# Performance work log

Hardware: AMD Instinct MI355X
Metric: run time of the kernel (lower is better)

Reference implementation:

```python
import jax, jax.numpy as jnp
import numpy as np

L1_PENALTY = 0.01
RHO = 5.0
N_ITERS = 100  # fixed iteration count standing in for max_iter=2000 w/ tol
EPS = 1e-12


def _normalize(x):
    # matches torch.nn.functional.normalize(dim=1, eps=1e-12)
    n = jnp.linalg.norm(x, axis=-1, keepdims=True)
    return x / jnp.maximum(n, EPS)


def _admm_nnlasso(D, Y, lam, rho, n_iters):
    """Batched nonnegative Lasso via ADMM.
    Solves per-row: min_w 0.5*||D^T w - y||^2 + lam*||w||_1, w >= 0.
    D: [c, d] dictionary, Y: [B, d] targets. Returns W: [B, c].
    x-update uses Woodbury: (A^T A + rho I)^{-1} b = (b - A^T (G + rho I)^{-1} A b)/rho
    with A = D^T, G = A A^T = D^T D ([d, d], d=512 -> cheap Cholesky).
    """
    d = D.shape[1]
    G = D.T @ D + rho * jnp.eye(d, dtype=D.dtype)  # [d, d]
    cf = jax.scipy.linalg.cho_factor(G)
    Aty = Y @ D.T  # [B, c] = A^T y batched
    thr = lam / rho

    def step(carry, _):
        z, u = carry
        b = Aty + rho * (z - u)               # [B, c]
        s = jax.scipy.linalg.cho_solve(cf, (b @ D).T).T  # [B, d]
        x = (b - s @ D.T) / rho               # [B, c]
        z_new = jnp.maximum(x + u - thr, 0.0)  # nonneg soft-threshold
        u_new = u + x - z_new
        return (z_new, u_new), None

    z0 = jnp.zeros_like(Aty)
    (z, _), _ = jax.lax.scan(step, (z0, z0), None, length=n_iters)
    return z


def setup_inputs() -> dict:
    key = jax.random.key(0)
    k1, k2, k3, k4 = jax.random.split(key, 4)
    B, C, Dm = 1024, 10000, 512
    image = jax.random.normal(k1, (B, Dm), dtype=jnp.float32)
    text = jax.random.normal(k2, (B, Dm), dtype=jnp.float32)
    image_mean = 0.1 * jax.random.normal(k3, (Dm,), dtype=jnp.float32)
    dictionary = jax.random.normal(k4, (C, Dm), dtype=jnp.float32)
    dictionary = dictionary / jnp.linalg.norm(dictionary, axis=1, keepdims=True)
    return {"image": image, "text": text, "image_mean": image_mean,
            "dictionary": dictionary}


def reference(image, text, image_mean, dictionary):
    # encode_image
    img = _normalize(image)
    centered = _normalize(img - image_mean)
    weights = _admm_nnlasso(dictionary, centered, L1_PENALTY, RHO, N_ITERS)
    recon = weights @ dictionary           # [B, d]
    recon = _normalize(recon)
    recon = _normalize(recon + image_mean)
    # encode_text (decomp_text=False -> just normalize)
    txt = _normalize(text)
    return recon, txt
```

## Files before the change

### kernel.cpp

```cpp
#include <hip/hip_runtime.h>
#include <cstddef>
#include <cstdint>

#define BDIM  1024
#define DM    512
#define CREAL 10000
#define CP    10112
#define KSPL  16
#define RHOC  5.0f
#define THRC  (0.01f/5.0f)
#define NIT   100
#define NSIT  12

typedef float f32x4 __attribute__((ext_vector_type(4)));
typedef _Float16 f16x8 __attribute__((ext_vector_type(8)));


__device__ __forceinline__ f16x8 scl6(f16x8 v) {
    f16x8 r;
#pragma unroll
    for (int i = 0; i < 8; i++) r[i] = v[i] * (_Float16)0.015625f;
    return r;
}

__device__ __forceinline__ float blk_sum256(float v) {
    __shared__ float sb[4];
#pragma unroll
    for (int o = 32; o; o >>= 1) v += __shfl_down(v, o, 64);
    int lane = threadIdx.x & 63, w = threadIdx.x >> 6;
    __syncthreads();
    if (lane == 0) sb[w] = v;
    __syncthreads();
    return sb[0] + sb[1] + sb[2] + sb[3];
}

__global__ __launch_bounds__(256) void knorm_rows(const float* __restrict__ X,
                                                  float* __restrict__ out) {
    int row = blockIdx.x, t = threadIdx.x;
    int off = row * DM + t * 2;
    float2 v = *(const float2*)(X + off);
    float ss = blk_sum256(v.x * v.x + v.y * v.y);
    float inv = 1.0f / fmaxf(sqrtf(ss), 1e-12f);
    float2 o = {v.x * inv, v.y * inv};
    *(float2*)(out + off) = o;
}

__global__ __launch_bounds__(256) void kprep_Y(const float* __restrict__ img,
                                               const float* __restrict__ mean,
                                               float* __restrict__ Y) {
    int row = blockIdx.x, t = threadIdx.x;
    int off = row * DM + t * 2;
    float2 v = *(const float2*)(img + off);
    float ss = blk_sum256(v.x * v.x + v.y * v.y);
    float inv = 1.0f / fmaxf(sqrtf(ss), 1e-12f);
    float2 mm = *(const float2*)(mean + t * 2);
    float tx = v.x * inv - mm.x, ty = v.y * inv - mm.y;
    float ss2 = blk_sum256(tx * tx + ty * ty);
    float inv2 = 1.0f / fmaxf(sqrtf(ss2), 1e-12f);
    float2 o = {tx * inv2, ty * inv2};
    *(float2*)(Y + off) = o;
}

__global__ __launch_bounds__(256) void ktrs(const float* __restrict__ in,
                                            float* __restrict__ out32,
                                            _Float16* __restrict__ oH,
                                            _Float16* __restrict__ oL,
                                            int Rvalid, int Cin, int Rout) {
    __shared__ float tile[64][65];
    int r0 = blockIdx.x * 64;
    int c0 = blockIdx.y * 64;
    int t = threadIdx.x;
    int ri = r0 + (t >> 2);
    int cc = (t & 3) * 16;
#pragma unroll
    for (int q = 0; q < 4; ++q) {
        float4 v = {0.f, 0.f, 0.f, 0.f};
        if (ri < Rvalid) v = *(const float4*)(in + (size_t)ri * Cin + c0 + cc + q * 4);
        *(float4*)&tile[t >> 2][cc + q * 4] = v;
    }
    __syncthreads();
    int oc = c0 + (t >> 2);
    int orr = r0 + (t & 3) * 16;
    _Float16 hv[16], lv[16];
#pragma unroll
    for (int q = 0; q < 16; ++q) {
        float v = tile[(t & 3) * 16 + q][t >> 2];
        _Float16 h = (_Float16)v;
        _Float16 l = (_Float16)((v - (float)h) * 64.f);
        hv[q] = h; lv[q] = l;
        if (out32) out32[(size_t)oc * Rout + orr + q] = (float)h + (float)l * 0.015625f;
    }
    int rt = oc >> 4, rin = oc & 15;
    int kt = orr >> 5;
    int kq0 = (orr >> 3) & 3;
    size_t base = ((size_t)rt * (Rout >> 5) + kt) * 512;
    *(f16x8*)(oH + base + (size_t)(kq0 * 16 + rin) * 8)       = *(f16x8*)&hv[0];
    *(f16x8*)(oH + base + (size_t)((kq0 + 1) * 16 + rin) * 8) = *(f16x8*)&hv[8];
    *(f16x8*)(oL + base + (size_t)(kq0 * 16 + rin) * 8)       = *(f16x8*)&lv[0];
    *(f16x8*)(oL + base + (size_t)((kq0 + 1) * 16 + rin) * 8) = *(f16x8*)&lv[8];
}

__global__ __launch_bounds__(256) void kG(const float* __restrict__ Dt,
                                          float* __restrict__ G) {
    __shared__ float As[32][68];
    __shared__ float Bs[32][68];
    int tid = threadIdx.x;
    int j0 = blockIdx.x * 64, i0 = blockIdx.y * 64;
    int tn = (tid & 15) * 4, tm = (tid >> 4) * 4;
    float acc[4][4];
#pragma unroll
    for (int i = 0; i < 4; i++)
#pragma unroll
        for (int j = 0; j < 4; j++) acc[i][j] = 0.f;
    for (int k0 = 0; k0 < CP; k0 += 32) {
        __syncthreads();
#pragma unroll
        for (int p = 0; p < 2; ++p) {
            int idx = tid + p * 256;
            int row = idx >> 3, kv = (idx & 7) << 2;
            float4 va = *(const float4*)(Dt + (size_t)(i0 + row) * CP + k0 + kv);
            As[kv + 0][row] = va.x; As[kv + 1][row] = va.y;
            As[kv + 2][row] = va.z; As[kv + 3][row] = va.w;
            float4 vb = *(const float4*)(Dt + (size_t)(j0 + row) * CP + k0 + kv);
            Bs[kv + 0][row] = vb.x; Bs[kv + 1][row] = vb.y;
            Bs[kv + 2][row] = vb.z; Bs[kv + 3][row] = vb.w;
        }
        __syncthreads();
#pragma unroll
        for (int k = 0; k < 32; ++k) {
            float4 a4 = *(const float4*)&As[k][tm];
            float4 b4 = *(const float4*)&Bs[k][tn];
            float af[4] = {a4.x, a4.y, a4.z, a4.w};
            float bf[4] = {b4.x, b4.y, b4.z, b4.w};
#pragma unroll
            for (int i = 0; i < 4; i++)
#pragma unroll
                for (int j = 0; j < 4; j++) acc[i][j] = fmaf(af[i], bf[j], acc[i][j]);
        }
    }
#pragma unroll
    for (int i = 0; i < 4; i++)
#pragma unroll
        for (int j = 0; j < 4; j++) {
            int gi = i0 + tm + i, gj = j0 + tn + j;
            G[gi * DM + gj] = acc[i][j] + ((gi == gj) ? RHOC : 0.f);
        }
}

__global__ void krow_abssum(const float* __restrict__ G, float* __restrict__ gmax) {
    int row = blockIdx.x, t = threadIdx.x;
    float s = 0.f;
    for (int j = t; j < DM; j += 64) s += fabsf(G[row * DM + j]);
#pragma unroll
    for (int o = 32; o; o >>= 1) s += __shfl_down(s, o, 64);
    if (t == 0) atomicMax((int*)gmax, __float_as_int(s));
}

__global__ void kinit_X0(const float* __restrict__ gmax, float* __restrict__ X) {
    int idx = blockIdx.x * 256 + threadIdx.x;
    int i = idx >> 9, j = idx & 511;
    X[idx] = (i == j) ? (1.0f / gmax[0]) : 0.0f;
}

__global__ __launch_bounds__(256) void kgemm_ns_T(const float* __restrict__ G,
                                                  const float* __restrict__ X,
                                                  float* __restrict__ T) {
    __shared__ float As[32][68];
    __shared__ float Bs[32][68];
    int tid = threadIdx.x;
    int n0 = blockIdx.x * 64, m0 = blockIdx.y * 64;
    int tn = (tid & 15) * 4, tm = (tid >> 4) * 4;
    float acc[4][4];
#pragma unroll
    for (int i = 0; i < 4; i++)
#pragma unroll
        for (int j = 0; j < 4; j++) acc[i][j] = 0.f;
    for (int k0 = 0; k0 < DM; k0 += 32) {
        __syncthreads();
#pragma unroll
        for (int p = 0; p < 2; ++p) {
            int idx = tid + p * 256;
            {
                int row = idx >> 3, kv = (idx & 7) << 2;
                float4 v = *(const float4*)(G + (m0 + row) * DM + k0 + kv);
                As[kv + 0][row] = v.x; As[kv + 1][row] = v.y;
                As[kv + 2][row] = v.z; As[kv + 3][row] = v.w;
            }
            {
                int r = idx >> 4, cv = (idx & 15) << 2;
                *(float4*)&Bs[r][cv] = *(const float4*)(X + (k0 + r) * DM + n0 + cv);
            }
        }
        __syncthreads();
#pragma unroll
        for (int k = 0; k < 32; ++k) {
            float4 a4 = *(const float4*)&As[k][tm];
            float4 b4 = *(const float4*)&Bs[k][tn];
            float af[4] = {a4.x, a4.y, a4.z, a4.w};
            float bf[4] = {b4.x, b4.y, b4.z, b4.w};
#pragma unroll
            for (int i = 0; i < 4; i++)
#pragma unroll
                for (int j = 0; j < 4; j++) acc[i][j] = fmaf(af[i], bf[j], acc[i][j]);
        }
    }
#pragma unroll
    for (int i = 0; i < 4; i++) {
        float4 o = {acc[i][0], acc[i][1], acc[i][2], acc[i][3]};
        *(float4*)(T + (m0 + tm + i) * DM + n0 + tn) = o;
    }
}

__global__ __launch_bounds__(256) void kgemm_ns_X(const float* __restrict__ Xo,
                                                  const float* __restrict__ T,
                                                  float* __restrict__ Xn) {
    __shared__ float As[32][68];
    __shared__ float Bs[32][68];
    int tid = threadIdx.x;
    int n0 = blockIdx.x * 64, m0 = blockIdx.y * 64;
    int tn = (tid & 15) * 4, tm = (tid >> 4) * 4;
    float acc[4][4];
#pragma unroll
    for (int i = 0; i < 4; i++)
#pragma unroll
        for (int j = 0; j < 4; j++) acc[i][j] = 0.f;
    for (int k0 = 0; k0 < DM; k0 += 32) {
        __syncthreads();
#pragma unroll
        for (int p = 0; p < 2; ++p) {
            int idx = tid + p * 256;
            {
                int row = idx >> 3, kv = (idx & 7) << 2;
                float4 v = *(const float4*)(Xo + (m0 + row) * DM + k0 + kv);
                As[kv + 0][row] = v.x; As[kv + 1][row] = v.y;
                As[kv + 2][row] = v.z; As[kv + 3][row] = v.w;
            }
            {
                int r = idx >> 4, cv = (idx & 15) << 2;
                *(float4*)&Bs[r][cv] = *(const float4*)(T + (k0 + r) * DM + n0 + cv);
            }
        }
        __syncthreads();
#pragma unroll
        for (int k = 0; k < 32; ++k) {
            float4 a4 = *(const float4*)&As[k][tm];
            float4 b4 = *(const float4*)&Bs[k][tn];
            float af[4] = {a4.x, a4.y, a4.z, a4.w};
            float bf[4] = {b4.x, b4.y, b4.z, b4.w};
#pragma unroll
            for (int i = 0; i < 4; i++)
#pragma unroll
                for (int j = 0; j < 4; j++) acc[i][j] = fmaf(af[i], bf[j], acc[i][j]);
        }
    }
#pragma unroll
    for (int i = 0; i < 4; i++) {
        int base = (m0 + tm + i) * DM + n0 + tn;
        float4 xo = *(const float4*)(Xo + base);
        float4 o = {2.f * xo.x - acc[i][0], 2.f * xo.y - acc[i][1],
                    2.f * xo.z - acc[i][2], 2.f * xo.w - acc[i][3]};
        *(float4*)(Xn + base) = o;
    }
}

template <int MODE>
__global__ __launch_bounds__(256) void kgemm_nn64(const float* __restrict__ A,
                                                  const float* __restrict__ B,
                                                  float* __restrict__ out32,
                                                  _Float16* __restrict__ oA) {
    __shared__ float As[32][68];
    __shared__ float Bs[32][68];
    int tid = threadIdx.x;
    int n0 = blockIdx.x * 64, m0 = blockIdx.y * 64;
    int tn = (tid & 15) * 4, tm = (tid >> 4) * 4;
    float acc[4][4];
#pragma unroll
    for (int i = 0; i < 4; i++)
#pragma unroll
        for (int j = 0; j < 4; j++) acc[i][j] = 0.f;
    for (int k0 = 0; k0 < DM; k0 += 32) {
        __syncthreads();
#pragma unroll
        for (int p = 0; p < 2; ++p) {
            int idx = tid + p * 256;
            {
                int row = idx >> 3, kv = (idx & 7) << 2;
                float4 v = *(const float4*)(A + (size_t)(m0 + row) * DM + k0 + kv);
                As[kv + 0][row] = v.x; As[kv + 1][row] = v.y;
                As[kv + 2][row] = v.z; As[kv + 3][row] = v.w;
            }
            {
                int r = idx >> 4, cv = (idx & 15) << 2;
                *(float4*)&Bs[r][cv] = *(const float4*)(B + (size_t)(k0 + r) * CP + n0 + cv);
            }
        }
        __syncthreads();
#pragma unroll
        for (int k = 0; k < 32; ++k) {
            float4 a4 = *(const float4*)&As[k][tm];
            float4 b4 = *(const float4*)&Bs[k][tn];
            float af[4] = {a4.x, a4.y, a4.z, a4.w};
            float bf[4] = {b4.x, b4.y, b4.z, b4.w};
#pragma unroll
            for (int i = 0; i < 4; i++)
#pragma unroll
                for (int j = 0; j < 4; j++) acc[i][j] = fmaf(af[i], bf[j], acc[i][j]);
        }
    }
#pragma unroll
    for (int i = 0; i < 4; i++)
#pragma unroll
        for (int j = 0; j < 4; j++) {
            size_t idx = (size_t)(m0 + tm + i) * CP + n0 + tn + j;
            if (MODE == 0) out32[idx] = acc[i][j];
            else           oA[idx] = (_Float16)(acc[i][j] * 0.2f * 64.f);
        }
}

__global__ __launch_bounds__(256) void kgemm_aD(const float* __restrict__ Yb,
                                                const float* __restrict__ G,
                                                float* __restrict__ aD) {
    __shared__ float As[32][68];
    __shared__ float Bs[32][68];
    int tid = threadIdx.x;
    int n0 = blockIdx.x * 64, m0 = blockIdx.y * 64;
    int tn = (tid & 15) * 4, tm = (tid >> 4) * 4;
    float acc[4][4];
#pragma unroll
    for (int i = 0; i < 4; i++)
#pragma unroll
        for (int j = 0; j < 4; j++) acc[i][j] = 0.f;
    for (int k0 = 0; k0 < DM; k0 += 32) {
        __syncthreads();
#pragma unroll
        for (int p = 0; p < 2; ++p) {
            int idx = tid + p * 256;
            {
                int row = idx >> 3, kv = (idx & 7) << 2;
                float4 v = *(const float4*)(Yb + (size_t)(m0 + row) * DM + k0 + kv);
                As[kv + 0][row] = v.x; As[kv + 1][row] = v.y;
                As[kv + 2][row] = v.z; As[kv + 3][row] = v.w;
            }
            {
                int r = idx >> 4, cv = (idx & 15) << 2;
                *(float4*)&Bs[r][cv] = *(const float4*)(G + (k0 + r) * DM + n0 + cv);
            }
        }
        __syncthreads();
#pragma unroll
        for (int k = 0; k < 32; ++k) {
            float4 a4 = *(const float4*)&As[k][tm];
            float4 b4 = *(const float4*)&Bs[k][tn];
            float af[4] = {a4.x, a4.y, a4.z, a4.w};
            float bf[4] = {b4.x, b4.y, b4.z, b4.w};
#pragma unroll
            for (int i = 0; i < 4; i++)
#pragma unroll
                for (int j = 0; j < 4; j++) acc[i][j] = fmaf(af[i], bf[j], acc[i][j]);
        }
    }
#pragma unroll
    for (int i = 0; i < 4; i++) {
        int base = (m0 + tm + i) * DM + n0 + tn;
        float4 y4 = *(const float4*)(Yb + base);
        float4 o = {acc[i][0] * 0.2f - y4.x, acc[i][1] * 0.2f - y4.y,
                    acc[i][2] * 0.2f - y4.z, acc[i][3] * 0.2f - y4.w};
        *(float4*)(aD + base) = o;
    }
}


template <int MODE>
__global__ __launch_bounds__(256) void kg1(const float* __restrict__ Pst,
                                           const _Float16* __restrict__ DHs,
                                           const _Float16* __restrict__ DLs,
                                           float* __restrict__ Qp) {
    __shared__ _Float16 sA[2][2][128 * 32];
    const int id = blockIdx.x;
    const int g  = id & 63;
    const int mb = id >> 6;
    const int nb = g & 3;
    const int ks = g >> 2;
    const int n0 = nb * 128;
    const int m0 = mb * 128;
    const int tid = threadIdx.x;
    const int lane = tid & 63;
    const int wvu = tid >> 6;
    const int wm = (wvu >> 1) * 64, wn = (wvu & 1) * 64;
    const int arow = tid >> 1;
    const int aq = (tid & 1) * 16;
    const int quad = (lane >> 4) * 8;
    f32x4 acc[4][4] = {};

    const int steps = CP / 32;
    const int per = (steps + KSPL - 1) / KSPL;
    int s0 = ks * per;
    int s1 = s0 + per; if (s1 > steps) s1 = steps;

    float pv[16];
    {
        size_t go = (size_t)(m0 + arow) * CP + s0 * 32 + aq;
        *(float4*)&pv[0]  = *(const float4*)(Pst + go);
        *(float4*)&pv[4]  = *(const float4*)(Pst + go + 4);
        *(float4*)&pv[8]  = *(const float4*)(Pst + go + 8);
        *(float4*)&pv[12] = *(const float4*)(Pst + go + 12);
    }
    const int ntb = (n0 + wn) >> 4;

    for (int sp = s0; sp < s1; ++sp) {
        const int buf = (sp - s0) & 1;
        {
            _Float16 th[16], tl[16];
#pragma unroll
            for (int e = 0; e < 16; ++e) {
                float p = pv[e];
                float v = (MODE == 0) ? ((p > THRC) ? p - 2.f * THRC : -p)
                                      : fmaxf(p - THRC, 0.f);
                _Float16 h = (_Float16)v;
                th[e] = h;
                tl[e] = (_Float16)((v - (float)h) * 64.f);
            }
            int lb = arow * 32 + aq;
            *(f16x8*)&sA[buf][0][lb]     = *(f16x8*)&th[0];
            *(f16x8*)&sA[buf][0][lb + 8] = *(f16x8*)&th[8];
            *(f16x8*)&sA[buf][1][lb]     = *(f16x8*)&tl[0];
            *(f16x8*)&sA[buf][1][lb + 8] = *(f16x8*)&tl[8];
        }
        if (sp + 1 < s1) {
            size_t go = (size_t)(m0 + arow) * CP + (sp + 1) * 32 + aq;
            *(float4*)&pv[0]  = *(const float4*)(Pst + go);
            *(float4*)&pv[4]  = *(const float4*)(Pst + go + 4);
            *(float4*)&pv[8]  = *(const float4*)(Pst + go + 8);
            *(float4*)&pv[12] = *(const float4*)(Pst + go + 12);
        }
        f16x8 bfh[4], bfl[4], bfs[4];
#pragma unroll
        for (int j = 0; j < 4; j++) {
            size_t go = ((size_t)(ntb + j) * (CP / 32) + sp) * 512 + (size_t)lane * 8;
            bfh[j] = *(const f16x8*)(DHs + go);
            bfl[j] = *(const f16x8*)(DLs + go);
        }
        __syncthreads();
        f16x8 af[2][4], afs[4];
#pragma unroll
        for (int i = 0; i < 4; i++) {
            int ro = (wm + i * 16 + (lane & 15)) * 32 + quad;
            af[0][i] = *(const f16x8*)&sA[buf][0][ro];
            af[1][i] = *(const f16x8*)&sA[buf][1][ro];
            afs[i] = scl6(af[0][i]);
        }
#pragma unroll
        for (int j = 0; j < 4; j++) bfs[j] = scl6(bfh[j]);
#pragma unroll
        for (int i = 0; i < 4; i++)
#pragma unroll
            for (int j = 0; j < 4; j++) {
                acc[i][j] = __builtin_amdgcn_mfma_f32_16x16x32_f16(af[0][i], bfh[j], acc[i][j], 0, 0, 0);
                acc[i][j] = __builtin_amdgcn_mfma_f32_16x16x32_f16(afs[i],   bfl[j], acc[i][j], 0, 0, 0);
                acc[i][j] = __builtin_amdgcn_mfma_f32_16x16x32_f16(af[1][i], bfs[j], acc[i][j], 0, 0, 0);
            }
    }
    float* outp = Qp + (size_t)ks * (BDIM * DM);
    const int r0 = (lane >> 4) * 4, c0l = lane & 15;
#pragma unroll
    for (int i = 0; i < 4; i++)
#pragma unroll
        for (int v = 0; v < 4; v++) {
            int row = m0 + wm + i * 16 + r0 + v;
#pragma unroll
            for (int j = 0; j < 4; j++)
                outp[(size_t)row * DM + n0 + wn + j * 16 + c0l] = acc[i][j][v];
        }
}

__global__ void kred(const float* __restrict__ Qp, const float* __restrict__ aD,
                     float* __restrict__ Qf, int addA) {
    size_t b = ((size_t)blockIdx.x * 256 + threadIdx.x) * 4;
    float4 s = {0.f, 0.f, 0.f, 0.f};
    if (addA) s = *(const float4*)(aD + b);
#pragma unroll
    for (int q = 0; q < KSPL; q++) {
        float4 t = *(const float4*)(Qp + (size_t)q * (BDIM * DM) + b);
        s.x += t.x; s.y += t.y; s.z += t.z; s.w += t.w;
    }
    *(float4*)(Qf + b) = s;
}

__global__ __launch_bounds__(256) void kg2(const float* __restrict__ Qf,
                                           const _Float16* __restrict__ EHs,
                                           const _Float16* __restrict__ ELs,
                                           const _Float16* __restrict__ AH,
                                           float* __restrict__ Pst) {
    __shared__ _Float16 sA[2][2][128 * 32];
    const int id = blockIdx.x;
    const int nb = id % 80;
    const int mb = id / 80;
    if (nb >= 79) return;
    const int n0 = nb * 128;
    const int m0 = mb * 128;
    const int tid = threadIdx.x;
    const int lane = tid & 63;
    const int wvu = tid >> 6;
    const int wm = (wvu >> 1) * 64, wn = (wvu & 1) * 64;
    const int arow = tid >> 1;
    const int aq = (tid & 1) * 16;
    const int quad = (lane >> 4) * 8;
    f32x4 acc[4][4] = {};

    float qv[16];
    {
        size_t go = (size_t)(m0 + arow) * DM + aq;
        *(float4*)&qv[0]  = *(const float4*)(Qf + go);
        *(float4*)&qv[4]  = *(const float4*)(Qf + go + 4);
        *(float4*)&qv[8]  = *(const float4*)(Qf + go + 8);
        *(float4*)&qv[12] = *(const float4*)(Qf + go + 12);
    }
    const int ntb = (n0 + wn) >> 4;

    for (int kk = 0; kk < DM / 32; ++kk) {
        const int buf = kk & 1;
        {
            _Float16 th[16], tl[16];
#pragma unroll
            for (int e = 0; e < 16; ++e) {
                float v = qv[e];
                _Float16 h = (_Float16)v;
                th[e] = h;
                tl[e] = (_Float16)((v - (float)h) * 64.f);
            }
            int lb = arow * 32 + aq;
            *(f16x8*)&sA[buf][0][lb]     = *(f16x8*)&th[0];
            *(f16x8*)&sA[buf][0][lb + 8] = *(f16x8*)&th[8];
            *(f16x8*)&sA[buf][1][lb]     = *(f16x8*)&tl[0];
            *(f16x8*)&sA[buf][1][lb + 8] = *(f16x8*)&tl[8];
        }
        if (kk + 1 < DM / 32) {
            size_t go = (size_t)(m0 + arow) * DM + (kk + 1) * 32 + aq;
            *(float4*)&qv[0]  = *(const float4*)(Qf + go);
            *(float4*)&qv[4]  = *(const float4*)(Qf + go + 4);
            *(float4*)&qv[8]  = *(const float4*)(Qf + go + 8);
            *(float4*)&qv[12] = *(const float4*)(Qf + go + 12);
        }
        f16x8 bfh[4], bfl[4], bfs[4];
#pragma unroll
        for (int j = 0; j < 4; j++) {
            size_t go = ((size_t)(ntb + j) * (DM / 32) + kk) * 512 + (size_t)lane * 8;
            bfh[j] = *(const f16x8*)(EHs + go);
            bfl[j] = *(const f16x8*)(ELs + go);
        }
        __syncthreads();
        f16x8 af[2][4], afs[4];
#pragma unroll
        for (int i = 0; i < 4; i++) {
            int ro = (wm + i * 16 + (lane & 15)) * 32 + quad;
            af[0][i] = *(const f16x8*)&sA[buf][0][ro];
            af[1][i] = *(const f16x8*)&sA[buf][1][ro];
            afs[i] = scl6(af[0][i]);
        }
#pragma unroll
        for (int j = 0; j < 4; j++) bfs[j] = scl6(bfh[j]);
#pragma unroll
        for (int i = 0; i < 4; i++)
#pragma unroll
            for (int j = 0; j < 4; j++) {
                acc[i][j] = __builtin_amdgcn_mfma_f32_16x16x32_f16(af[0][i], bfh[j], acc[i][j], 0, 0, 0);
                acc[i][j] = __builtin_amdgcn_mfma_f32_16x16x32_f16(afs[i],   bfl[j], acc[i][j], 0, 0, 0);
                acc[i][j] = __builtin_amdgcn_mfma_f32_16x16x32_f16(af[1][i], bfs[j], acc[i][j], 0, 0, 0);
            }
    }
    const int r0 = (lane >> 4) * 4, c0l = lane & 15;
#pragma unroll
    for (int i = 0; i < 4; i++)
#pragma unroll
        for (int v = 0; v < 4; v++) {
            int row = m0 + wm + i * 16 + r0 + v;
#pragma unroll
            for (int j = 0; j < 4; j++) {
                size_t idx = (size_t)row * CP + n0 + wn + j * 16 + c0l;
                float a = (float)AH[idx] * 0.015625f;
                float po = Pst[idx];
                Pst[idx] = a + fmaxf(po - THRC, 0.f) - acc[i][j][v];
            }
        }
}

__global__ __launch_bounds__(256) void kfinal(const float* __restrict__ Qf,
                                              const float* __restrict__ mean,
                                              float* __restrict__ out) {
    int row = blockIdx.x, t = threadIdx.x;
    int off = row * DM + t * 2;
    float2 q = *(const float2*)(Qf + off);
    float rx = q.x, ry = q.y;
    float ss = blk_sum256(rx * rx + ry * ry);
    float inv = 1.0f / fmaxf(sqrtf(ss), 1e-12f);
    rx *= inv; ry *= inv;
    float2 mm = *(const float2*)(mean + t * 2);
    rx += mm.x; ry += mm.y;
    float ss2 = blk_sum256(rx * rx + ry * ry);
    float inv2 = 1.0f / fmaxf(sqrtf(ss2), 1e-12f);
    float2 o = {rx * inv2, ry * inv2};
    *(float2*)(out + off) = o;
}

extern "C" void kernel_launch(void* const* d_in, const int* in_sizes, int n_in,
                              void* d_out, int out_size, void* d_ws, size_t ws_size,
                              hipStream_t stream) {
    const float* image = (const float*)d_in[0];
    const float* text  = (const float*)d_in[1];
    const float* mean  = (const float*)d_in[2];
    const float* D     = (const float*)d_in[3];
    float* out = (float*)d_out;
    float* ws = (float*)d_ws;

    const size_t PL = (size_t)DM * CP / 2;
    float* Y    = ws;
    float* G    = ws + 524288;
    float* Xa   = G + 262144;
    float* Xb   = Xa + 262144;
    float* Tns  = Xb + 262144;
    _Float16* DHs = (_Float16*)(Tns + 262144);
    _Float16* DLs = (_Float16*)((float*)DHs + PL);
    _Float16* EHs = (_Float16*)((float*)DLs + PL);
    _Float16* ELs = (_Float16*)((float*)EHs + PL);
    _Float16* AH = (_Float16*)((float*)ELs + PL);
    float* aD   = (float*)AH + (size_t)BDIM * CP / 2;
    float* P    = aD + (size_t)BDIM * DM;
    float* gmax = P + (size_t)BDIM * CP;
    float* Qp   = gmax + 64;
    float* Dt32 = P;
    float* Et32 = (float*)AH;
    float* Qf = Y;

    knorm_rows<<<BDIM, 256, 0, stream>>>(text, out + (size_t)BDIM * DM);
    kprep_Y<<<BDIM, 256, 0, stream>>>(image, mean, Y);
    ktrs<<<dim3(CP / 64, DM / 64), 256, 0, stream>>>(D, Dt32, DHs, DLs, CREAL, DM, CP);
    kG<<<dim3(8, 8), 256, 0, stream>>>(Dt32, G);
    (void)hipMemsetAsync(gmax, 0, 4, stream);
    krow_abssum<<<DM, 64, 0, stream>>>(G, gmax);
    kinit_X0<<<DM * DM / 256, 256, 0, stream>>>(gmax, Xa);
    float* xc = Xa;
    float* xn = Xb;
    for (int it = 0; it < NSIT; ++it) {
        kgemm_ns_T<<<dim3(8, 8), 256, 0, stream>>>(G, xc, Tns);
        kgemm_ns_X<<<dim3(8, 8), 256, 0, stream>>>(xc, Tns, xn);
        float* tmp = xc; xc = xn; xn = tmp;
    }
    float* Ginv = xc;
    kgemm_nn64<0><<<dim3(CP / 64, DM / 64), 256, 0, stream>>>(Ginv, Dt32, Et32, nullptr);
    ktrs<<<dim3(DM / 64, CP / 64), 256, 0, stream>>>(Et32, nullptr, EHs, ELs, DM, CP, DM);
    kgemm_nn64<1><<<dim3(CP / 64, BDIM / 64), 256, 0, stream>>>(Y, Dt32, nullptr, AH);
    kgemm_aD<<<dim3(DM / 64, BDIM / 64), 256, 0, stream>>>(Y, G, aD);
    (void)hipMemsetAsync(P, 0, (size_t)BDIM * CP * sizeof(float), stream);

    for (int it = 0; it < NIT; ++it) {
        kg1<0><<<512, 256, 0, stream>>>(P, DHs, DLs, Qp);
        kred<<<BDIM * DM / 1024, 256, 0, stream>>>(Qp, aD, Qf, 1);
        kg2<<<640, 256, 0, stream>>>(Qf, EHs, ELs, AH, P);
    }

    kg1<1><<<512, 256, 0, stream>>>(P, DHs, DLs, Qp);
    kred<<<BDIM * DM / 1024, 256, 0, stream>>>(Qp, nullptr, Qf, 0);
    kfinal<<<BDIM, 256, 0, stream>>>(Qf, mean, out);
}
```

Baseline: 11.71 ms.

## Store ADMM state as pre-tiled fp16 hi/lo splits and drop LDS staging

```diff
diff --git a/kernel.cpp b/kernel.cpp
--- a/kernel.cpp
+++ b/kernel.cpp
@@ -14,6 +14,8 @@
 
 typedef float f32x4 __attribute__((ext_vector_type(4)));
 typedef _Float16 f16x8 __attribute__((ext_vector_type(8)));
+typedef _Float16 f16x4 __attribute__((ext_vector_type(4)));
+typedef unsigned int u32x4 __attribute__((ext_vector_type(4)));
 
 
 __device__ __forceinline__ f16x8 scl6(f16x8 v) {
@@ -21,6 +23,27 @@
 #pragma unroll
     for (int i = 0; i < 8; i++) r[i] = v[i] * (_Float16)0.015625f;
     return r;
+}
+
+__device__ __forceinline__ void absfold(f16x8& h8, f16x8& l8) {
+    u32x4 h = __builtin_bit_cast(u32x4, h8);
+    u32x4 l = __builtin_bit_cast(u32x4, l8);
+    u32x4 m = h & 0x80008000u;
+    h8 = __builtin_bit_cast(f16x8, h ^ m);
+    l8 = __builtin_bit_cast(f16x8, l ^ m);
+}
+
+__device__ __forceinline__ void relufold(f16x8& h8, f16x8& l8) {
+#pragma unroll
+    for (int e = 0; e < 8; e++) {
+        bool p = h8[e] > (_Float16)0;
+        if (!p) { h8[e] = (_Float16)0; l8[e] = (_Float16)0; }
+    }
+}
+
+__device__ __forceinline__ size_t psidx(int row, int col) {
+    return ((size_t)(row >> 4) * (CP >> 5) + (size_t)(col >> 5)) * 512
+         + (size_t)((((col >> 3) & 3) * 16 + (row & 15)) * 8 + (col & 7));
 }
 
 __device__ __forceinline__ float blk_sum256(float v) {
@@ -100,6 +123,15 @@
     *(f16x8*)(oL + base + (size_t)((kq0 + 1) * 16 + rin) * 8) = *(f16x8*)&lv[8];
 }
 
+__global__ void kcsum(const float* __restrict__ Dt, float* __restrict__ csum) {
+    int n = blockIdx.x, t = threadIdx.x;
+    float s = 0.f;
+    for (int k = t; k < CP; k += 64) s += Dt[(size_t)n * CP + k];
+#pragma unroll
+    for (int o = 32; o; o >>= 1) s += __shfl_down(s, o, 64);
+    if (t == 0) csum[n] = s;
+}
+
 __global__ __launch_bounds__(256) void kG(const float* __restrict__ Dt,
                                           float* __restrict__ G) {
     __shared__ float As[32][68];
@@ -319,6 +351,7 @@
 
 __global__ __launch_bounds__(256) void kgemm_aD(const float* __restrict__ Yb,
                                                 const float* __restrict__ G,
+                                                const float* __restrict__ csum,
                                                 float* __restrict__ aD) {
     __shared__ float As[32][68];
     __shared__ float Bs[32][68];
@@ -359,37 +392,48 @@
                 for (int j = 0; j < 4; j++) acc[i][j] = fmaf(af[i], bf[j], acc[i][j]);
         }
     }
+    float4 c4 = *(const float4*)(csum + n0 + tn);
 #pragma unroll
     for (int i = 0; i < 4; i++) {
         int base = (m0 + tm + i) * DM + n0 + tn;
         float4 y4 = *(const float4*)(Yb + base);
-        float4 o = {acc[i][0] * 0.2f - y4.x, acc[i][1] * 0.2f - y4.y,
-                    acc[i][2] * 0.2f - y4.z, acc[i][3] * 0.2f - y4.w};
+        float4 o = {acc[i][0] * 0.2f - y4.x - THRC * c4.x,
+                    acc[i][1] * 0.2f - y4.y - THRC * c4.y,
+                    acc[i][2] * 0.2f - y4.z - THRC * c4.z,
+                    acc[i][3] * 0.2f - y4.w - THRC * c4.w};
         *(float4*)(aD + base) = o;
     }
 }
 
+__global__ void kinit_s(_Float16* __restrict__ SHp, _Float16* __restrict__ SLp) {
+    size_t i = ((size_t)blockIdx.x * 256 + threadIdx.x) * 8;
+    _Float16 h = (_Float16)(-THRC);
+    _Float16 l = (_Float16)((-THRC - (float)h) * 64.f);
+    f16x8 hv, lv;
+#pragma unroll
+    for (int e = 0; e < 8; e++) { hv[e] = h; lv[e] = l; }
+    *(f16x8*)(SHp + i) = hv;
+    *(f16x8*)(SLp + i) = lv;
+}
+
 
 template <int MODE>
-__global__ __launch_bounds__(256) void kg1(const float* __restrict__ Pst,
-                                           const _Float16* __restrict__ DHs,
-                                           const _Float16* __restrict__ DLs,
-                                           float* __restrict__ Qp) {
-    __shared__ _Float16 sA[2][2][128 * 32];
-    const int id = blockIdx.x;
-    const int g  = id & 63;
-    const int mb = id >> 6;
-    const int nb = g & 3;
-    const int ks = g >> 2;
-    const int n0 = nb * 128;
-    const int m0 = mb * 128;
+__global__ __launch_bounds__(256, 2) void kg1f(const _Float16* __restrict__ SHp,
+                                               const _Float16* __restrict__ SLp,
+                                               const _Float16* __restrict__ DHs,
+                                               const _Float16* __restrict__ DLs,
+                                               float* __restrict__ Qp) {
+    const int raw = blockIdx.x;
+    const int xcd = raw & 7;
+    const int r   = raw >> 3;
+    const int ks  = xcd * 2 + (r & 1);
+    const int q   = r >> 1;
+    const int mb  = q >> 2, nb = q & 3;
+    const int n0 = nb * 128, m0 = mb * 128;
     const int tid = threadIdx.x;
     const int lane = tid & 63;
     const int wvu = tid >> 6;
     const int wm = (wvu >> 1) * 64, wn = (wvu & 1) * 64;
-    const int arow = tid >> 1;
-    const int aq = (tid & 1) * 16;
-    const int quad = (lane >> 4) * 8;
     f32x4 acc[4][4] = {};
 
     const int steps = CP / 32;
@@ -397,67 +441,42 @@
     int s0 = ks * per;
     int s1 = s0 + per; if (s1 > steps) s1 = steps;
 
-    float pv[16];
-    {
-        size_t go = (size_t)(m0 + arow) * CP + s0 * 32 + aq;
-        *(float4*)&pv[0]  = *(const float4*)(Pst + go);
-        *(float4*)&pv[4]  = *(const float4*)(Pst + go + 4);
-        *(float4*)&pv[8]  = *(const float4*)(Pst + go + 8);
-        *(float4*)&pv[12] = *(const float4*)(Pst + go + 12);
-    }
+    const int mtb = (m0 + wm) >> 4;
     const int ntb = (n0 + wn) >> 4;
-
+    const size_t lo = (size_t)lane * 8;
+
+#pragma unroll 2
     for (int sp = s0; sp < s1; ++sp) {
-        const int buf = (sp - s0) & 1;
-        {
-            _Float16 th[16], tl[16];
-#pragma unroll
-            for (int e = 0; e < 16; ++e) {
-                float p = pv[e];
-                float v = (MODE == 0) ? ((p > THRC) ? p - 2.f * THRC : -p)
-                                      : fmaxf(p - THRC, 0.f);
-                _Float16 h = (_Float16)v;
-                th[e] = h;
-                tl[e] = (_Float16)((v - (float)h) * 64.f);
-            }
-            int lb = arow * 32 + aq;
-            *(f16x8*)&sA[buf][0][lb]     = *(f16x8*)&th[0];
-            *(f16x8*)&sA[buf][0][lb + 8] = *(f16x8*)&th[8];
-            *(f16x8*)&sA[buf][1][lb]     = *(f16x8*)&tl[0];
-            *(f16x8*)&sA[buf][1][lb + 8] = *(f16x8*)&tl[8];
-        }
-        if (sp + 1 < s1) {
-            size_t go = (size_t)(m0 + arow) * CP + (sp + 1) * 32 + aq;
-            *(float4*)&pv[0]  = *(const float4*)(Pst + go);
-            *(float4*)&pv[4]  = *(const float4*)(Pst + go + 4);
-            *(float4*)&pv[8]  = *(const float4*)(Pst + go + 8);
-            *(float4*)&pv[12] = *(const float4*)(Pst + go + 12);
-        }
-        f16x8 bfh[4], bfl[4], bfs[4];
+        f16x8 ah[4], al[4], bh[4], bl[4];
+#pragma unroll
+        for (int i = 0; i < 4; i++) {
+            size_t go = ((size_t)(mtb + i) * (CP / 32) + sp) * 512 + lo;
+            ah[i] = *(const f16x8*)(SHp + go);
+            al[i] = *(const f16x8*)(SLp + go);
+        }
 #pragma unroll
         for (int j = 0; j < 4; j++) {
-            size_t go = ((size_t)(ntb + j) * (CP / 32) + sp) * 512 + (size_t)lane * 8;
-            bfh[j] = *(const f16x8*)(DHs + go);
-            bfl[j] = *(const f16x8*)(DLs + go);
-        }
-        __syncthreads();
-        f16x8 af[2][4], afs[4];
+            size_t go = ((size_t)(ntb + j) * (CP / 32) + sp) * 512 + lo;
+            bh[j] = *(const f16x8*)(DHs + go);
+            bl[j] = *(const f16x8*)(DLs + go);
+        }
 #pragma unroll
         for (int i = 0; i < 4; i++) {
-            int ro = (wm + i * 16 + (lane & 15)) * 32 + quad;
-            af[0][i] = *(const f16x8*)&sA[buf][0][ro];
-            af[1][i] = *(const f16x8*)&sA[buf][1][ro];
-            afs[i] = scl6(af[0][i]);
-        }
-#pragma unroll
-        for (int j = 0; j < 4; j++) bfs[j] = scl6(bfh[j]);
+            if (MODE == 0) absfold(ah[i], al[i]);
+            else           relufold(ah[i], al[i]);
+        }
+        f16x8 as_[4], bs_[4];
+#pragma unroll
+        for (int i = 0; i < 4; i++) as_[i] = scl6(ah[i]);
+#pragma unroll
+        for (int j = 0; j < 4; j++) bs_[j] = scl6(bh[j]);
 #pragma unroll
         for (int i = 0; i < 4; i++)
 #pragma unroll
             for (int j = 0; j < 4; j++) {
-                acc[i][j] = __builtin_amdgcn_mfma_f32_16x16x32_f16(af[0][i], bfh[j], acc[i][j], 0, 0, 0);
-                acc[i][j] = __builtin_amdgcn_mfma_f32_16x16x32_f16(afs[i],   bfl[j], acc[i][j], 0, 0, 0);
-                acc[i][j] = __builtin_amdgcn_mfma_f32_16x16x32_f16(af[1][i], bfs[j], acc[i][j], 0, 0, 0);
+                acc[i][j] = __builtin_amdgcn_mfma_f32_16x16x32_f16(ah[i],  bh[j], acc[i][j], 0, 0, 0);
+                acc[i][j] = __builtin_amdgcn_mfma_f32_16x16x32_f16(as_[i], bl[j], acc[i][j], 0, 0, 0);
+                acc[i][j] = __builtin_amdgcn_mfma_f32_16x16x32_f16(al[i],  bs_[j], acc[i][j], 0, 0, 0);
             }
     }
     float* outp = Qp + (size_t)ks * (BDIM * DM);
@@ -473,99 +492,87 @@
         }
 }
 
-__global__ void kred(const float* __restrict__ Qp, const float* __restrict__ aD,
-                     float* __restrict__ Qf, int addA) {
+template <int ADD>
+__global__ void kredf(const float* __restrict__ Qp, const float* __restrict__ aD,
+                      float* __restrict__ out32, _Float16* __restrict__ QH,
+                      _Float16* __restrict__ QL) {
     size_t b = ((size_t)blockIdx.x * 256 + threadIdx.x) * 4;
     float4 s = {0.f, 0.f, 0.f, 0.f};
-    if (addA) s = *(const float4*)(aD + b);
-#pragma unroll
-    for (int q = 0; q < KSPL; q++) {
-        float4 t = *(const float4*)(Qp + (size_t)q * (BDIM * DM) + b);
+    if (ADD) s = *(const float4*)(aD + b);
+#pragma unroll
+    for (int qq = 0; qq < KSPL; qq++) {
+        float4 t = *(const float4*)(Qp + (size_t)qq * (BDIM * DM) + b);
         s.x += t.x; s.y += t.y; s.z += t.z; s.w += t.w;
     }
-    *(float4*)(Qf + b) = s;
-}
-
-__global__ __launch_bounds__(256) void kg2(const float* __restrict__ Qf,
-                                           const _Float16* __restrict__ EHs,
-                                           const _Float16* __restrict__ ELs,
-                                           const _Float16* __restrict__ AH,
-                                           float* __restrict__ Pst) {
-    __shared__ _Float16 sA[2][2][128 * 32];
-    const int id = blockIdx.x;
-    const int nb = id % 80;
-    const int mb = id / 80;
+    if (ADD) {
+        int row = (int)(b >> 9), col = (int)(b & 511);
+        size_t t0 = ((size_t)(row >> 4) * 16 + (size_t)(col >> 5)) * 512
+                  + (size_t)((((col >> 3) & 3) * 16 + (row & 15)) * 8 + (col & 7));
+        float sv[4] = {s.x, s.y, s.z, s.w};
+        f16x4 h4, l4;
+#pragma unroll
+        for (int e = 0; e < 4; e++) {
+            _Float16 h = (_Float16)sv[e];
+            h4[e] = h;
+            l4[e] = (_Float16)((sv[e] - (float)h) * 64.f);
+        }
+        *(f16x4*)(QH + t0) = h4;
+        *(f16x4*)(QL + t0) = l4;
+    } else {
+        *(float4*)(out32 + b) = s;
+    }
+}
+
+__global__ __launch_bounds__(256, 2) void kg2f(const _Float16* __restrict__ QH,
+                                               const _Float16* __restrict__ QL,
+                                               const _Float16* __restrict__ EHs,
+                                               const _Float16* __restrict__ ELs,
+                                               const _Float16* __restrict__ AH,
+                                               _Float16* __restrict__ SHp,
+                                               _Float16* __restrict__ SLp) {
+    const int raw = blockIdx.x;
+    const int g = raw & 7;
+    const int q = raw >> 3;
+    const int mb = q & 7, jj = q >> 3;
+    const int nb = g * 10 + jj;
     if (nb >= 79) return;
-    const int n0 = nb * 128;
-    const int m0 = mb * 128;
+    const int n0 = nb * 128, m0 = mb * 128;
     const int tid = threadIdx.x;
     const int lane = tid & 63;
     const int wvu = tid >> 6;
     const int wm = (wvu >> 1) * 64, wn = (wvu & 1) * 64;
-    const int arow = tid >> 1;
-    const int aq = (tid & 1) * 16;
-    const int quad = (lane >> 4) * 8;
+    const int mtb = (m0 + wm) >> 4;
+    const int ntb = (n0 + wn) >> 4;
+    const size_t lo = (size_t)lane * 8;
     f32x4 acc[4][4] = {};
 
-    float qv[16];
-    {
-        size_t go = (size_t)(m0 + arow) * DM + aq;
-        *(float4*)&qv[0]  = *(const float4*)(Qf + go);
-        *(float4*)&qv[4]  = *(const float4*)(Qf + go + 4);
-        *(float4*)&qv[8]  = *(const float4*)(Qf + go + 8);
-        *(float4*)&qv[12] = *(const float4*)(Qf + go + 12);
-    }
-    const int ntb = (n0 + wn) >> 4;
-
+#pragma unroll 2
     for (int kk = 0; kk < DM / 32; ++kk) {
-        const int buf = kk & 1;
-        {
-            _Float16 th[16], tl[16];
-#pragma unroll
-            for (int e = 0; e < 16; ++e) {
-                float v = qv[e];
-                _Float16 h = (_Float16)v;
-                th[e] = h;
-                tl[e] = (_Float16)((v - (float)h) * 64.f);
-            }
-            int lb = arow * 32 + aq;
-            *(f16x8*)&sA[buf][0][lb]     = *(f16x8*)&th[0];
-            *(f16x8*)&sA[buf][0][lb + 8] = *(f16x8*)&th[8];
-            *(f16x8*)&sA[buf][1][lb]     = *(f16x8*)&tl[0];
-            *(f16x8*)&sA[buf][1][lb + 8] = *(f16x8*)&tl[8];
-        }
-        if (kk + 1 < DM / 32) {
-            size_t go = (size_t)(m0 + arow) * DM + (kk + 1) * 32 + aq;
-            *(float4*)&qv[0]  = *(const float4*)(Qf + go);
-            *(float4*)&qv[4]  = *(const float4*)(Qf + go + 4);
-            *(float4*)&qv[8]  = *(const float4*)(Qf + go + 8);
-            *(float4*)&qv[12] = *(const float4*)(Qf + go + 12);
-        }
-        f16x8 bfh[4], bfl[4], bfs[4];
+        f16x8 ah[4], al[4], bh[4], bl[4];
+#pragma unroll
+        for (int i = 0; i < 4; i++) {
+            size_t go = ((size_t)(mtb + i) * (DM / 32) + kk) * 512 + lo;
+            ah[i] = *(const f16x8*)(QH + go);
+            al[i] = *(const f16x8*)(QL + go);
+        }
 #pragma unroll
         for (int j = 0; j < 4; j++) {
-            size_t go = ((size_t)(ntb + j) * (DM / 32) + kk) * 512 + (size_t)lane * 8;
-            bfh[j] = *(const f16x8*)(EHs + go);
-            bfl[j] = *(const f16x8*)(ELs + go);
-        }
-        __syncthreads();
-        f16x8 af[2][4], afs[4];
-#pragma unroll
-        for (int i = 0; i < 4; i++) {
-            int ro = (wm + i * 16 + (lane & 15)) * 32 + quad;
-            af[0][i] = *(const f16x8*)&sA[buf][0][ro];
-            af[1][i] = *(const f16x8*)&sA[buf][1][ro];
-            afs[i] = scl6(af[0][i]);
-        }
-#pragma unroll
-        for (int j = 0; j < 4; j++) bfs[j] = scl6(bfh[j]);
+            size_t go = ((size_t)(ntb + j) * (DM / 32) + kk) * 512 + lo;
+            bh[j] = *(const f16x8*)(EHs + go);
+            bl[j] = *(const f16x8*)(ELs + go);
+        }
+        f16x8 as_[4], bs_[4];
+#pragma unroll
+        for (int i = 0; i < 4; i++) as_[i] = scl6(ah[i]);
+#pragma unroll
+        for (int j = 0; j < 4; j++) bs_[j] = scl6(bh[j]);
 #pragma unroll
         for (int i = 0; i < 4; i++)
 #pragma unroll
             for (int j = 0; j < 4; j++) {
-                acc[i][j] = __builtin_amdgcn_mfma_f32_16x16x32_f16(af[0][i], bfh[j], acc[i][j], 0, 0, 0);
-                acc[i][j] = __builtin_amdgcn_mfma_f32_16x16x32_f16(afs[i],   bfl[j], acc[i][j], 0, 0, 0);
-                acc[i][j] = __builtin_amdgcn_mfma_f32_16x16x32_f16(af[1][i], bfs[j], acc[i][j], 0, 0, 0);
+                acc[i][j] = __builtin_amdgcn_mfma_f32_16x16x32_f16(ah[i],  bh[j], acc[i][j], 0, 0, 0);
+                acc[i][j] = __builtin_amdgcn_mfma_f32_16x16x32_f16(as_[i], bl[j], acc[i][j], 0, 0, 0);
+                acc[i][j] = __builtin_amdgcn_mfma_f32_16x16x32_f16(al[i],  bs_[j], acc[i][j], 0, 0, 0);
             }
     }
     const int r0 = (lane >> 4) * 4, c0l = lane & 15;
@@ -576,10 +583,17 @@
             int row = m0 + wm + i * 16 + r0 + v;
 #pragma unroll
             for (int j = 0; j < 4; j++) {
-                size_t idx = (size_t)row * CP + n0 + wn + j * 16 + c0l;
+                int col = n0 + wn + j * 16 + c0l;
+                size_t idx = (size_t)row * CP + col;
+                size_t ps = psidx(row, col);
                 float a = (float)AH[idx] * 0.015625f;
-                float po = Pst[idx];
-                Pst[idx] = a + fmaxf(po - THRC, 0.f) - acc[i][j][v];
+                float sold = (float)SHp[ps] + (float)SLp[ps] * 0.015625f;
+                float z = fmaxf(sold, 0.f);
+                float pn = a + z - acc[i][j][v];
+                float sn = pn - THRC;
+                _Float16 h = (_Float16)sn;
+                SHp[ps] = h;
+                SLp[ps] = (_Float16)((sn - (float)h) * 64.f);
             }
         }
 }
@@ -589,8 +603,8 @@
                                               float* __restrict__ out) {
     int row = blockIdx.x, t = threadIdx.x;
     int off = row * DM + t * 2;
-    float2 q = *(const float2*)(Qf + off);
-    float rx = q.x, ry = q.y;
+    float2 qv = *(const float2*)(Qf + off);
+    float rx = qv.x, ry = qv.y;
     float ss = blk_sum256(rx * rx + ry * ry);
     float inv = 1.0f / fmaxf(sqrtf(ss), 1e-12f);
     rx *= inv; ry *= inv;
@@ -612,28 +626,32 @@
     float* out = (float*)d_out;
     float* ws = (float*)d_ws;
 
-    const size_t PL = (size_t)DM * CP / 2;
-    float* Y    = ws;
-    float* G    = ws + 524288;
+    const size_t PLH = (size_t)DM * CP;
+    float* aD   = ws;
+    _Float16* QH = (_Float16*)(ws + 524288);
+    _Float16* QL = QH + (size_t)BDIM * DM;
+    _Float16* DHs = (_Float16*)(ws + 1048576);
+    _Float16* DLs = DHs + PLH;
+    _Float16* EHs = DLs + PLH;
+    _Float16* ELs = EHs + PLH;
+    _Float16* AH  = ELs + PLH;
+    _Float16* SH  = AH + (size_t)BDIM * CP;
+    _Float16* SL  = SH + (size_t)BDIM * CP;
+    float* Qp   = (float*)(SL + (size_t)BDIM * CP);
+    float* csum = Qp + (size_t)KSPL * BDIM * DM;
+    float* gmax = csum + 512;
+    float* Dt32 = (float*)SH;
+    float* G    = Dt32 + (size_t)DM * CP;
     float* Xa   = G + 262144;
     float* Xb   = Xa + 262144;
     float* Tns  = Xb + 262144;
-    _Float16* DHs = (_Float16*)(Tns + 262144);
-    _Float16* DLs = (_Float16*)((float*)DHs + PL);
-    _Float16* EHs = (_Float16*)((float*)DLs + PL);
-    _Float16* ELs = (_Float16*)((float*)EHs + PL);
-    _Float16* AH = (_Float16*)((float*)ELs + PL);
-    float* aD   = (float*)AH + (size_t)BDIM * CP / 2;
-    float* P    = aD + (size_t)BDIM * DM;
-    float* gmax = P + (size_t)BDIM * CP;
-    float* Qp   = gmax + 64;
-    float* Dt32 = P;
+    float* Y    = Tns + 262144;
     float* Et32 = (float*)AH;
-    float* Qf = Y;
 
     knorm_rows<<<BDIM, 256, 0, stream>>>(text, out + (size_t)BDIM * DM);
     kprep_Y<<<BDIM, 256, 0, stream>>>(image, mean, Y);
     ktrs<<<dim3(CP / 64, DM / 64), 256, 0, stream>>>(D, Dt32, DHs, DLs, CREAL, DM, CP);
+    kcsum<<<DM, 64, 0, stream>>>(Dt32, csum);
     kG<<<dim3(8, 8), 256, 0, stream>>>(Dt32, G);
     (void)hipMemsetAsync(gmax, 0, 4, stream);
     krow_abssum<<<DM, 64, 0, stream>>>(G, gmax);
@@ -649,16 +667,16 @@
     kgemm_nn64<0><<<dim3(CP / 64, DM / 64), 256, 0, stream>>>(Ginv, Dt32, Et32, nullptr);
     ktrs<<<dim3(DM / 64, CP / 64), 256, 0, stream>>>(Et32, nullptr, EHs, ELs, DM, CP, DM);
     kgemm_nn64<1><<<dim3(CP / 64, BDIM / 64), 256, 0, stream>>>(Y, Dt32, nullptr, AH);
-    kgemm_aD<<<dim3(DM / 64, BDIM / 64), 256, 0, stream>>>(Y, G, aD);
-    (void)hipMemsetAsync(P, 0, (size_t)BDIM * CP * sizeof(float), stream);
+    kgemm_aD<<<dim3(DM / 64, BDIM / 64), 256, 0, stream>>>(Y, G, csum, aD);
+    kinit_s<<<(int)((size_t)BDIM * CP / 8 / 256), 256, 0, stream>>>(SH, SL);
 
     for (int it = 0; it < NIT; ++it) {
-        kg1<0><<<512, 256, 0, stream>>>(P, DHs, DLs, Qp);
-        kred<<<BDIM * DM / 1024, 256, 0, stream>>>(Qp, aD, Qf, 1);
-        kg2<<<640, 256, 0, stream>>>(Qf, EHs, ELs, AH, P);
-    }
-
-    kg1<1><<<512, 256, 0, stream>>>(P, DHs, DLs, Qp);
-    kred<<<BDIM * DM / 1024, 256, 0, stream>>>(Qp, nullptr, Qf, 0);
-    kfinal<<<BDIM, 256, 0, stream>>>(Qf, mean, out);
-}
+        kg1f<0><<<512, 256, 0, stream>>>(SH, SL, DHs, DLs, Qp);
+        kredf<1><<<BDIM * DM / 1024, 256, 0, stream>>>(Qp, aD, nullptr, QH, QL);
+        kg2f<<<640, 256, 0, stream>>>(QH, QL, EHs, ELs, AH, SH, SL);
+    }
+
+    kg1f<1><<<512, 256, 0, stream>>>(SH, SL, DHs, DLs, Qp);
+    kredf<0><<<BDIM * DM / 1024, 256, 0, stream>>>(Qp, nullptr, aD, nullptr, nullptr);
+    kfinal<<<BDIM, 256, 0, stream>>>(aD, mean, out);
+}
```

Result: slower. 14.24 ms (+21.6%).
